# Performance work log

Measured on AMD Instinct MI355X. Metric: run time of the kernel, lower is better.

Reference implementation:

```python
import jax, jax.numpy as jnp
import numpy as np
from functools import partial

EDGES = [(1,2),(1,3),(1,4),(1,5),(1,6),(2,3),(2,7),(2,8),(3,4),(3,9),(4,5),(4,10),(5,6),(5,11),(6,12),(6,13),(7,8),(7,14),(8,9),(8,14),(9,10),(9,15),(10,11),(10,16),(11,12),(11,17),(12,13),(12,18),(13,18),(14,15),(14,19),(15,16),(15,19),(16,17),(16,20),(17,18),(17,21),(18,21),(19,20),(19,22),(20,21),(20,22),(21,22),(24,25),(24,29),(25,26),(25,29),(26,17),(26,30),(27,28),(27,31),(28,31),(29,30),(29,32),(30,31),(30,32),(31,32),(34,35),(34,39),(35,36),(35,39),(36,37),(36,30),(37,18),(37,41),(38,41),(39,40),(39,42),(30,41),(30,42),(31,42),(44,45),(44,49),(45,46),(45,49),(46,47),(46,50),(47,48),(47,51),(48,51),(49,50),(49,52),(50,51),(50,52),(51,52),(54,55),(54,59),(55,56),(55,59),(56,57),(56,60),(57,58),(57,61),(58,61),(59,60),(59,62),(50,61),(60,62),(61,62)]

B, C, T = 32, 64, 4000
F1, D, F2, NCLS = 8, 2, 16, 4
KLEN, GK = 64, 8


def _bn_pack(k, c):
    kg, kb = jax.random.split(k)
    g = jax.random.uniform(kg, (c,), minval=0.5, maxval=1.5)
    b = 0.1 * jax.random.normal(kb, (c,))
    return jnp.stack([g, b, jnp.zeros(c), jnp.ones(c)])  # gamma, beta, mean, var


def setup_inputs() -> dict:
    key = jax.random.key(0)
    ks = jax.random.split(key, 16)
    A = np.zeros((C, C), np.float32)
    for i, j in EDGES:
        A[i - 1, j - 1] = 1.0
        A[j - 1, i - 1] = 1.0
    np.fill_diagonal(A, 1.0)
    feat = F2 * ((T // 4 + 1) // 8)  # 16 * 125 = 2000
    s = 0.1
    return {
        "x": jax.random.normal(ks[0], (B, C, T), jnp.float32),
        "adjacency": jnp.asarray(A),
        "conv1_w": s * jax.random.normal(ks[1], (F1, 1, 1, KLEN), jnp.float32),
        "bnF1": jnp.stack([_bn_pack(jax.random.fold_in(ks[2], i), F1) for i in range(4)]),
        "imp": jax.random.normal(ks[3], (3, F1, C, C), jnp.float32),
        "gconv_w": s * jax.random.normal(ks[4], (3, F1, F1, 1, GK), jnp.float32),
        "dw_w": s * jax.random.normal(ks[5], (F1 * D, 1, C, 1), jnp.float32),
        "bn_sp": _bn_pack(ks[6], F1 * D),
        "sep_dw_w": s * jax.random.normal(ks[7], (F1 * D, 1, 1, 16), jnp.float32),
        "sep_pw_w": s * jax.random.normal(ks[8], (F2, F1 * D, 1, 1), jnp.float32),
        "bn_sep": _bn_pack(ks[9], F2),
        "fc_w": s * jax.random.normal(ks[10], (NCLS, feat), jnp.float32),
        "fc_b": jnp.zeros((NCLS,), jnp.float32),
    }


def _conv(x, w, pad, groups=1):
    return jax.lax.conv_general_dilated(
        x, w, (1, 1), pad, dimension_numbers=("NCHW", "OIHW", "NCHW"),
        feature_group_count=groups)


def _bn(x, p, eps=1e-3):
    g, b, m, v = p
    scale = g * jax.lax.rsqrt(v + eps)
    return x * scale[None, :, None, None] + (b - m * scale)[None, :, None, None]


def reference(x, adjacency, conv1_w, bnF1, imp, gconv_w, dw_w, bn_sp,
              sep_dw_w, sep_pw_w, bn_sep, fc_w, fc_b):
    Bv = x.shape[0]
    h = x[:, None, :, :]                                    # (B,1,C,T)
    h = _conv(h, conv1_w, [(0, 0), (31, 32)])                # 'same' for k=64
    h = _bn(h, bnF1[0])
    for l in range(3):                                       # GraphTemporalConvolution x3
        A = adjacency[None] * imp[l]                         # (F1,C,C) masked importance
        h = jnp.einsum("fcd,bfdt->bfct", A, h)
        h = _conv(h, gconv_w[l], [(0, 0), (3, 4)])           # 'same' for k=8
        h = jax.nn.elu(_bn(h, bnF1[l + 1]))
    # spatial depthwise conv with max-norm constraint (renorm, no grad through scale)
    norms = jnp.sqrt(jnp.sum(dw_w ** 2, axis=(1, 2, 3), keepdims=True))
    scale = jax.lax.stop_gradient(jnp.minimum(1.0, 1.0 / jnp.maximum(norms, 1e-7)))
    h = _conv(h, dw_w * scale, [(0, 0), (0, 0)], groups=F1)  # (B,F1*D,1,T)
    h = jax.nn.elu(_bn(h, bn_sp))
    h = h.reshape(Bv, F1 * D, 1, T // 4, 4).mean(-1)         # AvgPool (1,4)
    # separable conv
    h = _conv(h, sep_dw_w, [(0, 0), (8, 8)], groups=F1 * D)  # width T/4 + 1
    h = _conv(h, sep_pw_w, [(0, 0), (0, 0)])
    h = jax.nn.elu(_bn(h, bn_sep))
    W = h.shape[-1]
    Wp = (W // 8) * 8
    h = h[..., :Wp].reshape(Bv, F2, 1, Wp // 8, 8).mean(-1)  # AvgPool (1,8)
    feat = h.reshape(Bv, -1)
    return feat @ fc_w.T + fc_b
```

## Files before the change

### kernel.cpp

```cpp
#include <hip/hip_runtime.h>


#define B_   32
#define C_   64
#define T_   4000
#define F1_  8
#define TP_  1000
#define W2_  1001
#define MAXDEG 16
#define ROW4 130
#define ROWB 2080

typedef _Float16 h16x2 __attribute__((ext_vector_type(2)));
typedef _Float16 f16x8 __attribute__((ext_vector_type(8)));
typedef float    f32x4 __attribute__((ext_vector_type(4)));

static __device__ __forceinline__ float bf2f(unsigned short h) {
  union { unsigned int u; float f; } v; v.u = ((unsigned int)h) << 16; return v.f;
}
static __device__ __forceinline__ unsigned short f2bf(float f) {
  union { float f; unsigned int u; } v; v.f = f;
  unsigned int r = v.u + 0x7FFFu + ((v.u >> 16) & 1u);
  return (unsigned short)(r >> 16);
}
static __device__ __forceinline__ float lo_h(unsigned int u) {
  union { unsigned int u; _Float16 h[2]; } v; v.u = u; return (float)v.h[0];
}
static __device__ __forceinline__ float hi_h(unsigned int u) {
  union { unsigned int u; _Float16 h[2]; } v; v.u = u; return (float)v.h[1];
}
static __device__ __forceinline__ unsigned int pack2h(float a, float b) {
  union { _Float16 h[2]; unsigned int u; } v;
  v.h[0] = (_Float16)a; v.h[1] = (_Float16)b; return v.u;
}
static __device__ __forceinline__ h16x2 as_h2(unsigned int u) {
  union { unsigned int u; h16x2 h; } v; v.u = u; return v.h;
}
static __device__ __forceinline__ unsigned int alignb(unsigned int hi,
                                                      unsigned int lo,
                                                      unsigned int s) {
  return (unsigned int)(((((unsigned long long)hi) << 32) | lo) >> s);
}
#define PERM_LO(y, x) __builtin_amdgcn_perm((y), (x), 0x05040100u)
#define PERM_HI(y, x) __builtin_amdgcn_perm((y), (x), 0x07060302u)
#if defined(__has_builtin) && __has_builtin(__builtin_amdgcn_fdot2)
#define DOT2(a, b, c) __builtin_amdgcn_fdot2((a), (b), (c), false)
#else
static __device__ __forceinline__ float dot2_fb(h16x2 a, h16x2 b, float c) {
  return fmaf((float)a[0], (float)b[0], fmaf((float)a[1], (float)b[1], c));
}
#define DOT2(a, b, c) dot2_fb((a), (b), (c))
#endif
static __device__ __forceinline__ float eluf(float z) {
  return z > 0.0f ? z : __expf(z) - 1.0f;
}
static __device__ __forceinline__ float ldin(const void* p, int i, int isf32) {
  return isf32 ? ((const float*)p)[i] : bf2f(((const unsigned short*)p)[i]);
}

__global__ __launch_bounds__(256) void k0_setup(
    const void* __restrict__ adj, const void* __restrict__ imp,
    const void* __restrict__ dww, const void* __restrict__ w1,
    const void* __restrict__ bnF, const void* __restrict__ gw,
    const void* __restrict__ bnsp, const void* __restrict__ sdw,
    const void* __restrict__ pw, const void* __restrict__ bnsep,
    const void* __restrict__ fcw, const void* __restrict__ fcb,
    int* __restrict__ flag, int* __restrict__ deg, int* __restrict__ col,
    float* __restrict__ avals, unsigned int* __restrict__ w1h,
    uint4* __restrict__ wmf, float* __restrict__ dwn,
    float* __restrict__ sdwc, float* __restrict__ pwc,
    float* __restrict__ fcwc, float* __restrict__ fcbc,
    float* __restrict__ bnFs, float* __restrict__ bnsps,
    float* __restrict__ bnseps,
    unsigned int* __restrict__ avph,
    unsigned int* __restrict__ dwph)
{
  __shared__ float dwr[1024];
  __shared__ float dsc[16];
  int tid = threadIdx.x;
  int isf32 = (((const float*)adj)[0] == 1.0f) ? 1 : 0;
  if (tid == 0) *flag = isf32;

  for (int idx = tid; idx < 256; idx += 256) {
    int f = idx >> 5, p = idx & 31;
    w1h[idx] = pack2h(ldin(w1, f*64 + 2*p, isf32), ldin(w1, f*64 + 2*p + 1, isf32));
  }
  for (int idx = tid; idx < 384; idx += 256) {
    int lf = idx >> 6;
    int layer = lf >> 1, frag = lf & 1;
    int lane2 = idx & 63;
    int o = lane2 & 15, ii = (lane2 >> 4) + 4*frag;
    uint4 v; v.x = 0u; v.y = 0u; v.z = 0u; v.w = 0u;
    if (o < 8) {
      int bi = layer*512 + (o*8 + ii)*8;
      v.x = pack2h(ldin(gw, bi+0, isf32), ldin(gw, bi+1, isf32));
      v.y = pack2h(ldin(gw, bi+2, isf32), ldin(gw, bi+3, isf32));
      v.z = pack2h(ldin(gw, bi+4, isf32), ldin(gw, bi+5, isf32));
      v.w = pack2h(ldin(gw, bi+6, isf32), ldin(gw, bi+7, isf32));
    }
    wmf[idx] = v;
  }
  for (int i = tid; i < 256;  i += 256) sdwc[i] = ldin(sdw, i, isf32);
  for (int i = tid; i < 256;  i += 256) pwc[i]  = ldin(pw, i, isf32);
  for (int i = tid; i < 8000; i += 256) fcwc[i] = ldin(fcw, i, isf32);
  if (tid < 4) fcbc[tid] = ldin(fcb, tid, isf32);
  for (int i = tid; i < 1024; i += 256) dwr[i] = ldin(dww, i, isf32);

  if (tid < 64) {
    int c = tid, n = 0;
    for (int e = 0; e < MAXDEG; ++e) col[c*MAXDEG + e] = c;
    for (int d = 0; d < 64; ++d) {
      if (ldin(adj, c*64 + d, isf32) != 0.0f) {
        if (n < MAXDEG) col[c*MAXDEG + n] = d;
        ++n;
      }
    }
    deg[c] = n < MAXDEG ? n : MAXDEG;
  }
  __syncthreads();
  if (tid < 16) {
    float s2 = 0.0f;
    for (int c2 = 0; c2 < 64; ++c2) { float wv = dwr[tid*64 + c2]; s2 += wv*wv; }
    dsc[tid] = fminf(1.0f, 1.0f / fmaxf(sqrtf(s2), 1e-7f));
  }
  if (tid >= 64 && tid < 96) {
    int i = tid - 64, s = i >> 3, f = i & 7;
    float g = ldin(bnF, s*32 + f,      isf32);
    float b = ldin(bnF, s*32 + 8 + f,  isf32);
    float m = ldin(bnF, s*32 + 16 + f, isf32);
    float v = ldin(bnF, s*32 + 24 + f, isf32);
    float sc = g * rsqrtf(v + 1e-3f);
    bnFs[s*16 + f] = sc; bnFs[s*16 + 8 + f] = b - m*sc;
  }
  if (tid >= 96 && tid < 112) {
    int ch = tid - 96;
    float g = ldin(bnsp, ch, isf32), b = ldin(bnsp, 16 + ch, isf32);
    float m = ldin(bnsp, 32 + ch, isf32), v = ldin(bnsp, 48 + ch, isf32);
    float sc = g * rsqrtf(v + 1e-3f);
    bnsps[ch] = sc; bnsps[16 + ch] = b - m*sc;
  }
  if (tid >= 112 && tid < 128) {
    int ch = tid - 112;
    float g = ldin(bnsep, ch, isf32), b = ldin(bnsep, 16 + ch, isf32);
    float m = ldin(bnsep, 32 + ch, isf32), v = ldin(bnsep, 48 + ch, isf32);
    float sc = g * rsqrtf(v + 1e-3f);
    bnseps[ch] = sc; bnseps[16 + ch] = b - m*sc;
  }
  for (int combo = tid; combo < 3*8*64; combo += 256) {
    int l = combo >> 9, f = (combo >> 6) & 7, c = combo & 63;
    int dg = deg[c];
    for (int e = 0; e < MAXDEG; ++e) {
      float v = 0.0f;
      if (e < dg) {
        int d = col[c*MAXDEG + e];
        v = ldin(adj, c*64 + d, isf32) * ldin(imp, ((l*8 + f)*64 + c)*64 + d, isf32);
      }
      avals[((l*8 + f)*64 + c)*MAXDEG + e] = v;
    }
  }
  __syncthreads();
  for (int i = tid; i < 1024; i += 256) dwn[i] = dwr[i] * dsc[i >> 6];
  for (int idx = tid; idx < 3*8*64*8; idx += 256) {
    int base16 = (idx >> 3) * MAXDEG, p = idx & 7;
    avph[idx] = pack2h(avals[base16 + 2*p], avals[base16 + 2*p + 1]);
  }
  __syncthreads();
  for (int idx = tid; idx < 512; idx += 256) {
    int ch = idx >> 5, p = idx & 31;
    dwph[idx] = pack2h(dwn[ch*64 + 2*p], dwn[ch*64 + 2*p + 1]);
  }
}

__global__ __launch_bounds__(256, 4) void k1_conv1_bn(
    const void* __restrict__ x,
    const unsigned int* __restrict__ w1h,
    const float* __restrict__ bnFs,
    const int* __restrict__ flag,
    unsigned short* __restrict__ outp)
{
  __shared__ __align__(16) unsigned int xs[548];
  int tid = threadIdx.x;
  int bc = blockIdx.y;
  int b = bc >> 6, c = bc & 63;
  int tb = blockIdx.x * 1024;
  int isf32 = *flag;
  int row = bc * T_;
  if (isf32) {
    const float* xr = (const float*)x + row;
    for (int m = tid; m < 274; m += 256) {
      int tg = tb - 36 + 4*m;
      uint2 st;
      if (tg >= 0 && tg + 3 < T_) {
        float4 v = *(const float4*)(xr + tg);
        st.x = pack2h(v.x, v.y); st.y = pack2h(v.z, v.w);
      } else {
        float q0 = (tg   >= 0 && tg   < T_) ? xr[tg]   : 0.0f;
        float q1 = (tg+1 >= 0 && tg+1 < T_) ? xr[tg+1] : 0.0f;
        float q2 = (tg+2 >= 0 && tg+2 < T_) ? xr[tg+2] : 0.0f;
        float q3 = (tg+3 >= 0 && tg+3 < T_) ? xr[tg+3] : 0.0f;
        st.x = pack2h(q0, q1); st.y = pack2h(q2, q3);
      }
      *(uint2*)(xs + 2*m) = st;
    }
  } else {
    const unsigned short* xr = (const unsigned short*)x + row;
    for (int m = tid; m < 274; m += 256) {
      int tg = tb - 36 + 4*m;
      uint2 st;
      if (tg >= 0 && tg + 3 < T_) {
        uint2 v = *(const uint2*)(xr + tg);
        st.x = pack2h(bf2f((unsigned short)(v.x & 0xFFFFu)),
                      bf2f((unsigned short)(v.x >> 16)));
        st.y = pack2h(bf2f((unsigned short)(v.y & 0xFFFFu)),
                      bf2f((unsigned short)(v.y >> 16)));
      } else {
        float q0 = (tg   >= 0 && tg   < T_) ? bf2f(xr[tg])   : 0.0f;
        float q1 = (tg+1 >= 0 && tg+1 < T_) ? bf2f(xr[tg+1]) : 0.0f;
        float q2 = (tg+2 >= 0 && tg+2 < T_) ? bf2f(xr[tg+2]) : 0.0f;
        float q3 = (tg+3 >= 0 && tg+3 < T_) ? bf2f(xr[tg+3]) : 0.0f;
        st.x = pack2h(q0, q1); st.y = pack2h(q2, q3);
      }
      *(uint2*)(xs + 2*m) = st;
    }
  }
  __syncthreads();
  int t0 = tb + 4*tid;
  if (t0 >= T_) return;
  float acc[8][4];
  #pragma unroll
  for (int f = 0; f < 8; ++f)
    #pragma unroll
    for (int j = 0; j < 4; ++j) acc[f][j] = 0.0f;
  uint2 a0 = *(const uint2*)(xs + 2*tid + 2);
  uint2 a1 = *(const uint2*)(xs + 2*tid + 4);
  unsigned u0 = a0.x, u1 = a0.y, u2 = a1.x, u3 = a1.y;
  for (int cc = 0; cc < 16; ++cc) {
    unsigned od0 = alignb(u1, u0, 16);
    unsigned od1 = alignb(u2, u1, 16);
    unsigned od2 = alignb(u3, u2, 16);
    #pragma unroll
    for (int f = 0; f < 8; ++f) {
      h16x2 wa = as_h2(w1h[f*32 + 2*cc]);
      h16x2 wb = as_h2(w1h[f*32 + 2*cc + 1]);
      acc[f][0] = DOT2(as_h2(od0), wa, acc[f][0]);
      acc[f][0] = DOT2(as_h2(od1), wb, acc[f][0]);
      acc[f][1] = DOT2(as_h2(u1),  wa, acc[f][1]);
      acc[f][1] = DOT2(as_h2(u2),  wb, acc[f][1]);
      acc[f][2] = DOT2(as_h2(od1), wa, acc[f][2]);
      acc[f][2] = DOT2(as_h2(od2), wb, acc[f][2]);
      acc[f][3] = DOT2(as_h2(u2),  wa, acc[f][3]);
      acc[f][3] = DOT2(as_h2(u3),  wb, acc[f][3]);
    }
    u0 = u2; u1 = u3;
    if (cc < 15) {
      uint2 nx = *(const uint2*)(xs + 2*tid + 6 + 2*cc);
      u2 = nx.x; u3 = nx.y;
    }
  }
  #pragma unroll
  for (int f = 0; f < 8; ++f) {
    float sc = bnFs[f], sh = bnFs[8 + f];
    uint2 st;
    st.x = pack2h(acc[f][0]*sc + sh, acc[f][1]*sc + sh);
    st.y = pack2h(acc[f][2]*sc + sh, acc[f][3]*sc + sh);
    *(uint2*)(outp + ((b*8 + f)*64 + c)*T_ + t0) = st;
  }
}

__global__ __launch_bounds__(256, 6) void k23_gcn_gconv(
    const unsigned short* __restrict__ in,
    unsigned short* __restrict__ outp,
    const int* __restrict__ deg, const int* __restrict__ col,
    const float* __restrict__ avals,
    const unsigned int* __restrict__ avph,
    const uint4* __restrict__ wmf,
    const float* __restrict__ bnFs, int l)
{
  __shared__ __align__(16) uint4 ash[8 * ROW4];
  int tid = threadIdx.x;
  int wgid = blockIdx.y * 4 + blockIdx.x;
  int swz  = (wgid & 7) * 1024 + (wgid >> 3);
  int c = swz & 63;
  int xt = (swz >> 6) & 3;
  int b = swz >> 8;
  int tb = xt * 1024;
  int wb = tb - 8;
  int dg = deg[c];
  const int* cp = col + c*MAXDEG;

  {
    int i = tid >> 5;
    int mlane = tid & 31;
    int dgp = (dg + 1) >> 1;
    const unsigned int* wpp = avph + ((l*8 + i)*64 + c) * 8;
    const float* av = avals + ((l*8 + i)*64 + c) * MAXDEG;
    const unsigned short* rbp = in + (size_t)((b*8 + i) * 64) * T_;
    for (int m = mlane; m < ROW4; m += 32) {
      int t = wb + 8*m;
      float a[8] = {0,0,0,0,0,0,0,0};
      if (t >= 0 && t + 7 < T_) {
        for (int p = 0; p < dgp; ++p) {
          int d0 = cp[2*p];
          int d1 = cp[2*p + 1];
          h16x2 w2 = as_h2(wpp[p]);
          uint4 v0 = *(const uint4*)(rbp + d0*T_ + t);
          uint4 v1 = *(const uint4*)(rbp + d1*T_ + t);
          a[0] = DOT2(as_h2(PERM_LO(v1.x, v0.x)), w2, a[0]);
          a[1] = DOT2(as_h2(PERM_HI(v1.x, v0.x)), w2, a[1]);
          a[2] = DOT2(as_h2(PERM_LO(v1.y, v0.y)), w2, a[2]);
          a[3] = DOT2(as_h2(PERM_HI(v1.y, v0.y)), w2, a[3]);
          a[4] = DOT2(as_h2(PERM_LO(v1.z, v0.z)), w2, a[4]);
          a[5] = DOT2(as_h2(PERM_HI(v1.z, v0.z)), w2, a[5]);
          a[6] = DOT2(as_h2(PERM_LO(v1.w, v0.w)), w2, a[6]);
          a[7] = DOT2(as_h2(PERM_HI(v1.w, v0.w)), w2, a[7]);
        }
      } else if (t + 7 >= 0 && t < T_) {
        for (int e = 0; e < dg; ++e) {
          int d = cp[e];
          float wv = av[e];
          const unsigned short* rp = rbp + d*T_;
          #pragma unroll
          for (int q = 0; q < 8; ++q) {
            int tq = t + q;
            if (tq >= 0 && tq < T_)
              a[q] = fmaf(wv, lo_h((unsigned int)rp[tq]), a[q]);
          }
        }
      }
      uint4 o;
      o.x = pack2h(a[0], a[1]); o.y = pack2h(a[2], a[3]);
      o.z = pack2h(a[4], a[5]); o.w = pack2h(a[6], a[7]);
      ash[i*ROW4 + m] = o;
    }
  }
  __syncthreads();

  int lane = tid & 63;
  int wv4 = tid >> 6;
  int m = lane & 15, q = lane >> 4;
  union { uint4 u; f16x8 h; } w0u, w1u;
  w0u.u = wmf[(l*2 + 0)*64 + lane];
  w1u.u = wmf[(l*2 + 1)*64 + lane];
  int o8 = (m < 8) ? m : 0;
  float sc  = bnFs[(l+1)*16 + o8];
  float shb = bnFs[(l+1)*16 + 8 + o8];
  int Sm = m + 5;
  unsigned shv = ((unsigned)Sm & 1u) * 16u;
  int base4 = q*ROWB + ((2*Sm) & ~3);
  const char* ashc = (const char*)ash;
  const unsigned int* p0 =
      (const unsigned int*)(ashc + base4 + wv4*512);
  const unsigned int* p1 =
      (const unsigned int*)(ashc + base4 + wv4*512 + 4*ROWB);
  unsigned short* orow = outp + (size_t)((b*8 + o8)*64 + c) * T_;
  #pragma unroll
  for (int tile = 0; tile < 16; ++tile) {
    int nb = tile * 8;
    unsigned dwa[5], dwb[5];
    #pragma unroll
    for (int j2 = 0; j2 < 5; ++j2) {
      dwa[j2] = p0[nb + j2];
      dwb[j2] = p1[nb + j2];
    }
    union { unsigned d[4]; f16x8 h; } A0, A1;
    #pragma unroll
    for (int j = 0; j < 4; ++j) {
      A0.d[j] = alignb(dwa[j+1], dwa[j], shv);
      A1.d[j] = alignb(dwb[j+1], dwb[j], shv);
    }
    f32x4 acc = {0.0f, 0.0f, 0.0f, 0.0f};
    acc = __builtin_amdgcn_mfma_f32_16x16x32_f16(A0.h, w0u.h, acc, 0, 0, 0);
    acc = __builtin_amdgcn_mfma_f32_16x16x32_f16(A1.h, w1u.h, acc, 0, 0, 0);
    int t0g = tb + wv4*256 + tile*16 + 4*q;
    if (m < 8 && t0g < T_) {
      float e0 = eluf(acc[0]*sc + shb);
      float e1 = eluf(acc[1]*sc + shb);
      float e2 = eluf(acc[2]*sc + shb);
      float e3 = eluf(acc[3]*sc + shb);
      uint2 st; st.x = pack2h(e0, e1); st.y = pack2h(e2, e3);
      *(uint2*)(orow + t0g) = st;
    }
  }
}

__global__ __launch_bounds__(256) void k4_dw(
    const unsigned short* __restrict__ in,
    const unsigned int* __restrict__ dwph,
    const float* __restrict__ bnsps,
    float* __restrict__ p1)
{
  int tid = threadIdx.x;
  int bg = blockIdx.y;
  int b = bg >> 3, g = bg & 7;
  int tile = blockIdx.x * 256 + tid;
  if (tile >= 500) return;
  int t0 = tile * 8;
  int base = bg * (64 * T_);
  const unsigned int* w0pp = dwph + (2*g)*32;
  const unsigned int* w1pp = dwph + (2*g + 1)*32;
  float a0[8] = {0,0,0,0,0,0,0,0}, a1[8] = {0,0,0,0,0,0,0,0};
  for (int p = 0; p < 32; ++p) {
    h16x2 w02 = as_h2(w0pp[p]);
    h16x2 w12 = as_h2(w1pp[p]);
    uint4 v0 = *(const uint4*)(in + base + (2*p)*T_ + t0);
    uint4 v1 = *(const uint4*)(in + base + (2*p + 1)*T_ + t0);
    unsigned pr;
    pr = PERM_LO(v1.x, v0.x);
    a0[0] = DOT2(as_h2(pr), w02, a0[0]); a1[0] = DOT2(as_h2(pr), w12, a1[0]);
    pr = PERM_HI(v1.x, v0.x);
    a0[1] = DOT2(as_h2(pr), w02, a0[1]); a1[1] = DOT2(as_h2(pr), w12, a1[1]);
    pr = PERM_LO(v1.y, v0.y);
    a0[2] = DOT2(as_h2(pr), w02, a0[2]); a1[2] = DOT2(as_h2(pr), w12, a1[2]);
    pr = PERM_HI(v1.y, v0.y);
    a0[3] = DOT2(as_h2(pr), w02, a0[3]); a1[3] = DOT2(as_h2(pr), w12, a1[3]);
    pr = PERM_LO(v1.z, v0.z);
    a0[4] = DOT2(as_h2(pr), w02, a0[4]); a1[4] = DOT2(as_h2(pr), w12, a1[4]);
    pr = PERM_HI(v1.z, v0.z);
    a0[5] = DOT2(as_h2(pr), w02, a0[5]); a1[5] = DOT2(as_h2(pr), w12, a1[5]);
    pr = PERM_LO(v1.w, v0.w);
    a0[6] = DOT2(as_h2(pr), w02, a0[6]); a1[6] = DOT2(as_h2(pr), w12, a1[6]);
    pr = PERM_HI(v1.w, v0.w);
    a0[7] = DOT2(as_h2(pr), w02, a0[7]); a1[7] = DOT2(as_h2(pr), w12, a1[7]);
  }
  float sc0 = bnsps[2*g],     sh0 = bnsps[16 + 2*g];
  float sc1 = bnsps[2*g + 1], sh1 = bnsps[16 + 2*g + 1];
  int oi = t0 >> 2;
  float2 r0, r1;
  r0.x = 0.25f * (eluf(a0[0]*sc0+sh0) + eluf(a0[1]*sc0+sh0)
                + eluf(a0[2]*sc0+sh0) + eluf(a0[3]*sc0+sh0));
  r0.y = 0.25f * (eluf(a0[4]*sc0+sh0) + eluf(a0[5]*sc0+sh0)
                + eluf(a0[6]*sc0+sh0) + eluf(a0[7]*sc0+sh0));
  r1.x = 0.25f * (eluf(a1[0]*sc1+sh1) + eluf(a1[1]*sc1+sh1)
                + eluf(a1[2]*sc1+sh1) + eluf(a1[3]*sc1+sh1));
  r1.y = 0.25f * (eluf(a1[4]*sc1+sh1) + eluf(a1[5]*sc1+sh1)
                + eluf(a1[6]*sc1+sh1) + eluf(a1[7]*sc1+sh1));
  *(float2*)(p1 + (b*16 + 2*g)*TP_ + oi)     = r0;
  *(float2*)(p1 + (b*16 + 2*g + 1)*TP_ + oi) = r1;
}

__global__ __launch_bounds__(256) void k5_sep(
    const float* __restrict__ p1,
    const float* __restrict__ sdwc,
    const float* __restrict__ pwc,
    const float* __restrict__ bnseps,
    float* __restrict__ p2)
{
  __shared__ float ps[16*272];
  int tid = threadIdx.x;
  int wq = blockIdx.x, b = blockIdx.y;
  int wb = wq * 256;
  for (int ch = 0; ch < 16; ++ch) {
    for (int s = tid; s < 272; s += 256) {
      int t = wb - 8 + s;
      ps[ch*272 + s] = (t >= 0 && t < TP_) ? p1[(b*16 + ch)*TP_ + t] : 0.0f;
    }
  }
  __syncthreads();
  int w0 = wb + tid;
  if (w0 >= W2_) return;
  float dws[16];
  for (int ch = 0; ch < 16; ++ch) {
    float a = 0.0f;
    #pragma unroll
    for (int k = 0; k < 16; ++k)
      a = fmaf(sdwc[ch*16 + k], ps[ch*272 + tid + k], a);
    dws[ch] = a;
  }
  for (int f = 0; f < 16; ++f) {
    float a = 0.0f;
    #pragma unroll
    for (int ch = 0; ch < 16; ++ch) a = fmaf(pwc[f*16 + ch], dws[ch], a);
    float sc = bnseps[f], sh = bnseps[16 + f];
    p2[(b*16 + f)*W2_ + w0] = eluf(a*sc + sh);
  }
}

__global__ __launch_bounds__(256) void k6_fc(
    const float* __restrict__ p2,
    const float* __restrict__ fcwc,
    const float* __restrict__ fcbc,
    const int* __restrict__ flag,
    void* __restrict__ outp)
{
  __shared__ float red[4*256];
  int tid = threadIdx.x;
  int b = blockIdx.x;
  float part[4] = {0.0f, 0.0f, 0.0f, 0.0f};
  for (int idx = tid; idx < 2000; idx += 256) {
    int f = idx / 125, q = idx - f*125;
    const float* src = p2 + (b*16 + f)*W2_ + q*8;
    float s = src[0]+src[1]+src[2]+src[3]+src[4]+src[5]+src[6]+src[7];
    float mval = 0.125f * s;
    #pragma unroll
    for (int n = 0; n < 4; ++n) part[n] = fmaf(fcwc[n*2000 + idx], mval, part[n]);
  }
  #pragma unroll
  for (int n = 0; n < 4; ++n) red[n*256 + tid] = part[n];
  __syncthreads();
  for (int s = 128; s > 0; s >>= 1) {
    if (tid < s) {
      #pragma unroll
      for (int n = 0; n < 4; ++n) red[n*256 + tid] += red[n*256 + tid + s];
    }
    __syncthreads();
  }
  if (tid < 4) {
    float val = red[tid*256] + fcbc[tid];
    if (*flag) ((float*)outp)[b*4 + tid] = val;
    else       ((unsigned short*)outp)[b*4 + tid] = f2bf(val);
  }
}

extern "C" void kernel_launch(void* const* d_in, const int* in_sizes, int n_in,
                              void* d_out, int out_size, void* d_ws, size_t ws_size,
                              hipStream_t stream) {
  const void* x     = d_in[0];
  const void* adj   = d_in[1];
  const void* w1    = d_in[2];
  const void* bnF   = d_in[3];
  const void* imp   = d_in[4];
  const void* gw    = d_in[5];
  const void* dww   = d_in[6];
  const void* bnsp  = d_in[7];
  const void* sdw   = d_in[8];
  const void* pw    = d_in[9];
  const void* bnsep = d_in[10];
  const void* fcw   = d_in[11];
  const void* fcb   = d_in[12];

  char* w = (char*)d_ws;
  const size_t OFF = 262144000;
  unsigned short* bufA = (unsigned short*)(w);
  unsigned short* bufB = (unsigned short*)(w + 131072000);
  int*   flag   = (int*)  (w + OFF + 0);
  int*   deg    = (int*)  (w + OFF + 256);
  int*   col    = (int*)  (w + OFF + 512);
  float* avals  = (float*)(w + OFF + 4608);
  float* dwn    = (float*)(w + OFF + 108032);
  float* sdwc   = (float*)(w + OFF + 112128);
  float* pwc    = (float*)(w + OFF + 113152);
  float* fcwc   = (float*)(w + OFF + 114176);
  float* fcbc   = (float*)(w + OFF + 146176);
  float* bnFs   = (float*)(w + OFF + 146432);
  float* bnsps  = (float*)(w + OFF + 146688);
  float* bnseps = (float*)(w + OFF + 146944);
  float* p1     = (float*)(w + OFF + 147200);
  float* p2     = (float*)(w + OFF + 2195200);
  uint4* wmf    = (uint4*)(w + OFF + 4245248);
  unsigned int* avph = (unsigned int*)(w + OFF + 4251392);
  unsigned int* dwph = (unsigned int*)(w + OFF + 4300544);
  unsigned int* w1h  = (unsigned int*)(w + OFF + 4302592);

  k0_setup<<<1, 256, 0, stream>>>(adj, imp, dww, w1, bnF, gw, bnsp, sdw, pw,
                                  bnsep, fcw, fcb, flag, deg, col, avals,
                                  w1h, wmf, dwn, sdwc, pwc, fcwc, fcbc,
                                  bnFs, bnsps, bnseps, avph, dwph);
  k1_conv1_bn<<<dim3(4, B_*C_), 256, 0, stream>>>(x, w1h, bnFs, flag, bufA);
  for (int l = 0; l < 3; ++l) {
    const unsigned short* src = (l & 1) ? bufB : bufA;
    unsigned short*       dst = (l & 1) ? bufA : bufB;
    k23_gcn_gconv<<<dim3(4, B_*C_), 256, 0, stream>>>(src, dst, deg, col,
                                                      avals, avph, wmf, bnFs, l);
  }
  k4_dw<<<dim3(2, B_*F1_), 256, 0, stream>>>(bufB, dwph, bnsps, p1);
  k5_sep<<<dim3(4, B_), 256, 0, stream>>>(p1, sdwc, pwc, bnseps, p2);
  k6_fc<<<32, 256, 0, stream>>>(p2, fcwc, fcbc, flag, d_out);
}
```

Before: 545.4 us.

## Use all MFMA output rows via even/odd split and swizzle, pkrtz conversions

The gconv MFMA stage in the GCN kernel now computes even and odd time positions as two separate MFMA accumulations. Lanes with m>=8 previously held wasted rows; a ds_swizzle now moves results so every lane writes output. This halves the tile loop count and drops the variable-shift align on the A operand. Float-to-half packing also switches to the cvt_pkrtz builtin, which rounds toward zero instead of to nearest, a small precision change.

```diff
diff --git a/kernel.cpp b/kernel.cpp
--- a/kernel.cpp
+++ b/kernel.cpp
@@ -9,11 +9,12 @@
 #define W2_  1001
 #define MAXDEG 16
 #define ROW4 130
-#define ROWB 2080
+#define ROWD 520
 
 typedef _Float16 h16x2 __attribute__((ext_vector_type(2)));
 typedef _Float16 f16x8 __attribute__((ext_vector_type(8)));
 typedef float    f32x4 __attribute__((ext_vector_type(4)));
+typedef __fp16   cvt16x2 __attribute__((ext_vector_type(2)));
 
 static __device__ __forceinline__ float bf2f(unsigned short h) {
   union { unsigned int u; float f; } v; v.u = ((unsigned int)h) << 16; return v.f;
@@ -26,13 +27,21 @@
 static __device__ __forceinline__ float lo_h(unsigned int u) {
   union { unsigned int u; _Float16 h[2]; } v; v.u = u; return (float)v.h[0];
 }
-static __device__ __forceinline__ float hi_h(unsigned int u) {
-  union { unsigned int u; _Float16 h[2]; } v; v.u = u; return (float)v.h[1];
-}
 static __device__ __forceinline__ unsigned int pack2h(float a, float b) {
   union { _Float16 h[2]; unsigned int u; } v;
   v.h[0] = (_Float16)a; v.h[1] = (_Float16)b; return v.u;
 }
+#if defined(__has_builtin) && __has_builtin(__builtin_amdgcn_cvt_pkrtz)
+static __device__ __forceinline__ unsigned int pkh(float a, float b) {
+  union { cvt16x2 h; unsigned int u; } v;
+  v.h = __builtin_amdgcn_cvt_pkrtz(a, b);
+  return v.u;
+}
+#else
+static __device__ __forceinline__ unsigned int pkh(float a, float b) {
+  return pack2h(a, b);
+}
+#endif
 static __device__ __forceinline__ h16x2 as_h2(unsigned int u) {
   union { unsigned int u; h16x2 h; } v; v.u = u; return v.h;
 }
@@ -40,6 +49,11 @@
                                                       unsigned int lo,
                                                       unsigned int s) {
   return (unsigned int)(((((unsigned long long)hi) << 32) | lo) >> s);
+}
+static __device__ __forceinline__ float swz8(float v) {
+  union { float f; int i; } a; a.f = v;
+  a.i = __builtin_amdgcn_ds_swizzle(a.i, 0x201F);
+  return a.f;
 }
 #define PERM_LO(y, x) __builtin_amdgcn_perm((y), (x), 0x05040100u)
 #define PERM_HI(y, x) __builtin_amdgcn_perm((y), (x), 0x07060302u)
@@ -192,13 +206,13 @@
       uint2 st;
       if (tg >= 0 && tg + 3 < T_) {
         float4 v = *(const float4*)(xr + tg);
-        st.x = pack2h(v.x, v.y); st.y = pack2h(v.z, v.w);
+        st.x = pkh(v.x, v.y); st.y = pkh(v.z, v.w);
       } else {
         float q0 = (tg   >= 0 && tg   < T_) ? xr[tg]   : 0.0f;
         float q1 = (tg+1 >= 0 && tg+1 < T_) ? xr[tg+1] : 0.0f;
         float q2 = (tg+2 >= 0 && tg+2 < T_) ? xr[tg+2] : 0.0f;
         float q3 = (tg+3 >= 0 && tg+3 < T_) ? xr[tg+3] : 0.0f;
-        st.x = pack2h(q0, q1); st.y = pack2h(q2, q3);
+        st.x = pkh(q0, q1); st.y = pkh(q2, q3);
       }
       *(uint2*)(xs + 2*m) = st;
     }
@@ -209,16 +223,16 @@
       uint2 st;
       if (tg >= 0 && tg + 3 < T_) {
         uint2 v = *(const uint2*)(xr + tg);
-        st.x = pack2h(bf2f((unsigned short)(v.x & 0xFFFFu)),
-                      bf2f((unsigned short)(v.x >> 16)));
-        st.y = pack2h(bf2f((unsigned short)(v.y & 0xFFFFu)),
-                      bf2f((unsigned short)(v.y >> 16)));
+        st.x = pkh(bf2f((unsigned short)(v.x & 0xFFFFu)),
+                   bf2f((unsigned short)(v.x >> 16)));
+        st.y = pkh(bf2f((unsigned short)(v.y & 0xFFFFu)),
+                   bf2f((unsigned short)(v.y >> 16)));
       } else {
         float q0 = (tg   >= 0 && tg   < T_) ? bf2f(xr[tg])   : 0.0f;
         float q1 = (tg+1 >= 0 && tg+1 < T_) ? bf2f(xr[tg+1]) : 0.0f;
         float q2 = (tg+2 >= 0 && tg+2 < T_) ? bf2f(xr[tg+2]) : 0.0f;
         float q3 = (tg+3 >= 0 && tg+3 < T_) ? bf2f(xr[tg+3]) : 0.0f;
-        st.x = pack2h(q0, q1); st.y = pack2h(q2, q3);
+        st.x = pkh(q0, q1); st.y = pkh(q2, q3);
       }
       *(uint2*)(xs + 2*m) = st;
     }
@@ -261,8 +275,8 @@
   for (int f = 0; f < 8; ++f) {
     float sc = bnFs[f], sh = bnFs[8 + f];
     uint2 st;
-    st.x = pack2h(acc[f][0]*sc + sh, acc[f][1]*sc + sh);
-    st.y = pack2h(acc[f][2]*sc + sh, acc[f][3]*sc + sh);
+    st.x = pkh(acc[f][0]*sc + sh, acc[f][1]*sc + sh);
+    st.y = pkh(acc[f][2]*sc + sh, acc[f][3]*sc + sh);
     *(uint2*)(outp + ((b*8 + f)*64 + c)*T_ + t0) = st;
   }
 }
@@ -328,8 +342,8 @@
         }
       }
       uint4 o;
-      o.x = pack2h(a[0], a[1]); o.y = pack2h(a[2], a[3]);
-      o.z = pack2h(a[4], a[5]); o.w = pack2h(a[6], a[7]);
+      o.x = pkh(a[0], a[1]); o.y = pkh(a[2], a[3]);
+      o.z = pkh(a[4], a[5]); o.w = pkh(a[6], a[7]);
       ash[i*ROW4 + m] = o;
     }
   }
@@ -338,46 +352,52 @@
   int lane = tid & 63;
   int wv4 = tid >> 6;
   int m = lane & 15, q = lane >> 4;
+  int sel = (m >> 3) & 1;
   union { uint4 u; f16x8 h; } w0u, w1u;
   w0u.u = wmf[(l*2 + 0)*64 + lane];
   w1u.u = wmf[(l*2 + 1)*64 + lane];
-  int o8 = (m < 8) ? m : 0;
+  int o8 = m & 7;
   float sc  = bnFs[(l+1)*16 + o8];
   float shb = bnFs[(l+1)*16 + 8 + o8];
-  int Sm = m + 5;
-  unsigned shv = ((unsigned)Sm & 1u) * 16u;
-  int base4 = q*ROWB + ((2*Sm) & ~3);
-  const char* ashc = (const char*)ash;
-  const unsigned int* p0 =
-      (const unsigned int*)(ashc + base4 + wv4*512);
-  const unsigned int* p1 =
-      (const unsigned int*)(ashc + base4 + wv4*512 + 4*ROWB);
+  const unsigned int* ashd = (const unsigned int*)ash;
+  const unsigned int* p0 = ashd + q*ROWD + wv4*128 + m + 2;
+  const unsigned int* p1 = p0 + 4*ROWD;
   unsigned short* orow = outp + (size_t)((b*8 + o8)*64 + c) * T_;
   #pragma unroll
-  for (int tile = 0; tile < 16; ++tile) {
-    int nb = tile * 8;
+  for (int s = 0; s < 8; ++s) {
     unsigned dwa[5], dwb[5];
     #pragma unroll
-    for (int j2 = 0; j2 < 5; ++j2) {
-      dwa[j2] = p0[nb + j2];
-      dwb[j2] = p1[nb + j2];
-    }
-    union { unsigned d[4]; f16x8 h; } A0, A1;
+    for (int j = 0; j < 5; ++j) {
+      dwa[j] = p0[16*s + j];
+      dwb[j] = p1[16*s + j];
+    }
+    union { unsigned d[4]; f16x8 h; } Ae0, Ao0, Ae1, Ao1;
     #pragma unroll
     for (int j = 0; j < 4; ++j) {
-      A0.d[j] = alignb(dwa[j+1], dwa[j], shv);
-      A1.d[j] = alignb(dwb[j+1], dwb[j], shv);
-    }
-    f32x4 acc = {0.0f, 0.0f, 0.0f, 0.0f};
-    acc = __builtin_amdgcn_mfma_f32_16x16x32_f16(A0.h, w0u.h, acc, 0, 0, 0);
-    acc = __builtin_amdgcn_mfma_f32_16x16x32_f16(A1.h, w1u.h, acc, 0, 0, 0);
-    int t0g = tb + wv4*256 + tile*16 + 4*q;
-    if (m < 8 && t0g < T_) {
-      float e0 = eluf(acc[0]*sc + shb);
-      float e1 = eluf(acc[1]*sc + shb);
-      float e2 = eluf(acc[2]*sc + shb);
-      float e3 = eluf(acc[3]*sc + shb);
-      uint2 st; st.x = pack2h(e0, e1); st.y = pack2h(e2, e3);
+      Ao0.d[j] = dwa[j+1];
+      Ae0.d[j] = alignb(dwa[j+1], dwa[j], 16);
+      Ao1.d[j] = dwb[j+1];
+      Ae1.d[j] = alignb(dwb[j+1], dwb[j], 16);
+    }
+    f32x4 ae = {0.0f, 0.0f, 0.0f, 0.0f};
+    f32x4 ao = {0.0f, 0.0f, 0.0f, 0.0f};
+    ae = __builtin_amdgcn_mfma_f32_16x16x32_f16(Ae0.h, w0u.h, ae, 0, 0, 0);
+    ae = __builtin_amdgcn_mfma_f32_16x16x32_f16(Ae1.h, w1u.h, ae, 0, 0, 0);
+    ao = __builtin_amdgcn_mfma_f32_16x16x32_f16(Ao0.h, w0u.h, ao, 0, 0, 0);
+    ao = __builtin_amdgcn_mfma_f32_16x16x32_f16(Ao1.h, w1u.h, ao, 0, 0, 0);
+    float r0 = swz8(ae[2]);
+    float r1 = swz8(ao[2]);
+    float r2 = swz8(ae[3]);
+    float r3 = swz8(ao[3]);
+    float y0 = sel ? r0 : ae[0];
+    float y1 = sel ? r1 : ao[0];
+    float y2 = sel ? r2 : ae[1];
+    float y3 = sel ? r3 : ao[1];
+    int t0g = tb + wv4*256 + s*32 + 8*q + 4*sel;
+    if (t0g < T_) {
+      uint2 st;
+      st.x = pkh(eluf(y0*sc + shb), eluf(y1*sc + shb));
+      st.y = pkh(eluf(y2*sc + shb), eluf(y3*sc + shb));
       *(uint2*)(orow + t0g) = st;
     }
   }
```

Result: faster. 514.1 us (-5.7%).
